# Optimization experiments

Hardware: AMD Instinct MI355X
Metric: run time of the kernel (lower is better)

The kernel has to match this reference:

```python
import jax, jax.numpy as jnp
import numpy as np

EPS = 1e-5

def layernorm(x, w, b):
    mu = jnp.mean(x, axis=-1, keepdims=True)
    xc = x - mu
    var = jnp.mean(xc * xc, axis=-1, keepdims=True)
    return xc * jax.lax.rsqrt(var + EPS) * w + b

def setup_inputs() -> dict:
    key = jax.random.key(0)
    ks = jax.random.split(key, 9)
    B, T, Nm, Nl = 8, 8, 1024, 64
    Vw, Tw, H, Dh = 1024, 2048, 8, 64
    inner = H * Dh  # 512
    s_q = 1.0 / np.sqrt(Tw)
    s_kv = 1.0 / np.sqrt(Vw)
    s_o = 1.0 / np.sqrt(inner)
    return {
        "x": jax.random.normal(ks[0], (B, T, Nm, Vw), jnp.float32),
        "latents": jax.random.normal(ks[1], (B, T, Nl, Tw), jnp.float32),
        "nm_w": jnp.ones((Vw,), jnp.float32),
        "nm_b": jnp.zeros((Vw,), jnp.float32),
        "nl_w": jnp.ones((Tw,), jnp.float32),
        "nl_b": jnp.zeros((Tw,), jnp.float32),
        "Wq": jax.random.normal(ks[2], (Tw, inner), jnp.float32) * s_q,
        "Wkv": jax.random.normal(ks[3], (Vw, 2 * inner), jnp.float32) * s_kv,
        "Wout": jax.random.normal(ks[4], (inner, Tw), jnp.float32) * s_o,
    }

def reference(x, latents, nm_w, nm_b, nl_w, nl_b, Wq, Wkv, Wout):
    H, Dh = 8, 64
    scale = Dh ** (-0.5)
    B, T, Nm, _ = x.shape
    Nl = latents.shape[2]
    xn = layernorm(x, nm_w, nm_b)          # (B,T,Nm,Vw)
    ln = layernorm(latents, nl_w, nl_b)    # (B,T,Nl,Tw)
    q = (ln @ Wq).reshape(B, T, Nl, H, Dh)           # b t i h d
    kv = xn @ Wkv                                     # (B,T,Nm,2*inner)
    k, v = jnp.split(kv, 2, axis=-1)
    k = k.reshape(B, T, Nm, H, Dh)                    # b t j h d
    v = v.reshape(B, T, Nm, H, Dh)
    sim = jnp.einsum('btihd,btjhd->bthij', q * scale, k)  # (B,T,H,Nl,Nm)
    attn = jax.nn.softmax(sim, axis=-1)
    out = jnp.einsum('bthij,btjhd->btihd', attn, v)       # (B,T,Nl,H,Dh)
    out = out.reshape(B, T, Nl, H * Dh)
    return out @ Wout                                     # (B,T,Nl,Tw)
```

## Files before the change

kernel.cpp:

```cpp
#include <hip/hip_runtime.h>

typedef __attribute__((ext_vector_type(8))) short bfrag8;
typedef __attribute__((ext_vector_type(4))) float f32x4;

typedef const unsigned int __attribute__((address_space(1)))* gas1_u32;
typedef unsigned int __attribute__((address_space(3)))* gas3_u32;

#define DEV __device__ __forceinline__

DEV unsigned short f2bf(float f) {
  unsigned int u = __builtin_bit_cast(unsigned int, f);
  u += 0x7fffu + ((u >> 16) & 1u);
  return (unsigned short)(u >> 16);
}

DEV void gload_lds16(const void* g, void* l) {
  __builtin_amdgcn_global_load_lds((gas1_u32)g, (gas3_u32)l, 16, 0, 0);
}

__global__ __launch_bounds__(256) void k_xstats(
    const float* __restrict__ x, unsigned short* __restrict__ xb,
    float* __restrict__ mu, float* __restrict__ rstd)
{
  const int wid = threadIdx.x >> 6, lane = threadIdx.x & 63;
  const int row = blockIdx.x * 4 + wid;
  const float* base = x + (size_t)row * 1024;
  float4 v[4];
  #pragma unroll
  for (int i = 0; i < 4; ++i) v[i] = ((const float4*)base)[i * 64 + lane];
  float s = 0.f, q = 0.f;
  #pragma unroll
  for (int i = 0; i < 4; ++i) {
    s += v[i].x + v[i].y + v[i].z + v[i].w;
    q += v[i].x*v[i].x + v[i].y*v[i].y + v[i].z*v[i].z + v[i].w*v[i].w;
  }
  #pragma unroll
  for (int off = 32; off >= 1; off >>= 1) { s += __shfl_xor(s, off); q += __shfl_xor(q, off); }
  const float m  = s * (1.0f/1024.0f);
  const float var = q * (1.0f/1024.0f) - m * m;
  const float rs = rsqrtf(var + 1e-5f);
  if (lane == 0) { mu[row] = m; rstd[row] = rs; }
  unsigned short* ob = xb + (size_t)row * 1024;
  #pragma unroll
  for (int i = 0; i < 4; ++i) {
    ushort4 o;
    o.x = f2bf(v[i].x); o.y = f2bf(v[i].y); o.z = f2bf(v[i].z); o.w = f2bf(v[i].w);
    ((ushort4*)ob)[i * 64 + lane] = o;
  }
}

__global__ __launch_bounds__(256) void k_lnlat(
    const float* __restrict__ lat, const float* __restrict__ w,
    const float* __restrict__ b, unsigned short* __restrict__ ln)
{
  const int row = blockIdx.x, tid = threadIdx.x;
  const float* base = lat + (size_t)row * 2048;
  const float4 v0 = ((const float4*)base)[tid];
  const float4 v1 = ((const float4*)base)[256 + tid];
  float s = v0.x+v0.y+v0.z+v0.w + v1.x+v1.y+v1.z+v1.w;
  float q = v0.x*v0.x+v0.y*v0.y+v0.z*v0.z+v0.w*v0.w
          + v1.x*v1.x+v1.y*v1.y+v1.z*v1.z+v1.w*v1.w;
  #pragma unroll
  for (int off = 32; off >= 1; off >>= 1) { s += __shfl_xor(s, off); q += __shfl_xor(q, off); }
  __shared__ float red[8];
  const int wid = tid >> 6, lane = tid & 63;
  if (lane == 0) { red[wid] = s; red[4 + wid] = q; }
  __syncthreads();
  s = red[0] + red[1] + red[2] + red[3];
  q = red[4] + red[5] + red[6] + red[7];
  const float m  = s * (1.0f/2048.0f);
  const float var = q * (1.0f/2048.0f) - m * m;
  const float rs = rsqrtf(var + 1e-5f);
  const float4 w0 = ((const float4*)w)[tid], w1 = ((const float4*)w)[256 + tid];
  const float4 b0 = ((const float4*)b)[tid], b1 = ((const float4*)b)[256 + tid];
  ushort4 o0, o1;
  o0.x = f2bf((v0.x - m) * rs * w0.x + b0.x);
  o0.y = f2bf((v0.y - m) * rs * w0.y + b0.y);
  o0.z = f2bf((v0.z - m) * rs * w0.z + b0.z);
  o0.w = f2bf((v0.w - m) * rs * w0.w + b0.w);
  o1.x = f2bf((v1.x - m) * rs * w1.x + b1.x);
  o1.y = f2bf((v1.y - m) * rs * w1.y + b1.y);
  o1.z = f2bf((v1.z - m) * rs * w1.z + b1.z);
  o1.w = f2bf((v1.w - m) * rs * w1.w + b1.w);
  ((ushort4*)(ln + (size_t)row * 2048))[tid] = o0;
  ((ushort4*)(ln + (size_t)row * 2048))[256 + tid] = o1;
}

__global__ __launch_bounds__(256) void k_transpose_cast(
    const float* __restrict__ src, unsigned short* __restrict__ dst,
    int K, int N, const float* __restrict__ rowscale, float scale)
{
  __shared__ float tile[32][33];
  const int tx = threadIdx.x & 31, ty = threadIdx.x >> 5;
  const int ntiles = N >> 5;
  const int k0 = (blockIdx.x / ntiles) << 5;
  const int n0 = (blockIdx.x % ntiles) << 5;
  #pragma unroll
  for (int r = 0; r < 4; ++r) {
    const int kk = ty + r * 8;
    float v = src[(size_t)(k0 + kk) * N + n0 + tx] * scale;
    if (rowscale) v *= rowscale[k0 + kk];
    tile[kk][tx] = v;
  }
  __syncthreads();
  #pragma unroll
  for (int r = 0; r < 4; ++r) {
    const int nn = ty + r * 8;
    dst[(size_t)(n0 + nn) * K + k0 + tx] = f2bf(tile[tx][nn]);
  }
}

__global__ __launch_bounds__(256) void k_c1c2_part(
    const float* __restrict__ Wkv, const float* __restrict__ w,
    const float* __restrict__ b, float* __restrict__ part)
{
  const int kc = blockIdx.x;
  const int n  = blockIdx.y * 256 + threadIdx.x;
  float s1 = 0.f, s2 = 0.f;
  const int k0 = kc * 64;
  for (int k = k0; k < k0 + 64; ++k) {
    const float wv = Wkv[(size_t)k * 1024 + n];
    s1 += w[k] * wv;
    s2 += b[k] * wv;
  }
  part[(size_t)(kc * 2 + 0) * 1024 + n] = s1;
  part[(size_t)(kc * 2 + 1) * 1024 + n] = s2;
}

__global__ __launch_bounds__(256) void k_c1c2_red(
    const float* __restrict__ part, float* __restrict__ c1, float* __restrict__ c2)
{
  const int n = blockIdx.x * 256 + threadIdx.x;
  float s1 = 0.f, s2 = 0.f;
  #pragma unroll
  for (int kc = 0; kc < 16; ++kc) {
    s1 += part[(size_t)(kc * 2 + 0) * 1024 + n];
    s2 += part[(size_t)(kc * 2 + 1) * 1024 + n];
  }
  c1[n] = s1; c2[n] = s2;
}

template<int BM, int BN, int BK, int WM, int WN, int NT, int MODE>
__global__ __launch_bounds__(NT, 2) void k_gemm(
    const unsigned short* __restrict__ A, int lda,
    const unsigned short* __restrict__ Bt, int ldb,
    int Mb, int K, int mtiles, int ntiles,
    void* __restrict__ Cout, int ldc,
    const float* __restrict__ mu, const float* __restrict__ rstd,
    const float* __restrict__ c1, const float* __restrict__ c2)
{
  static_assert(BK == 64, "staging/swizzle assumes BK=64 (128B rows)");
  constexpr int NW = NT / 64;
  constexpr int MF = (BM / WM) / 16;
  constexpr int NF = (BN / WN) / 16;
  constexpr int KS = BK / 32;
  constexpr int LA = (BM * BK) / (8 * NT);
  constexpr int LB = (BN * BK) / (8 * NT);
  static_assert(WM * WN == NW, "wave grid");

  __shared__ __attribute__((aligned(16))) unsigned short As0[BM * BK];
  __shared__ __attribute__((aligned(16))) unsigned short As1[BM * BK];
  __shared__ __attribute__((aligned(16))) unsigned short Bs0[BN * BK];
  __shared__ __attribute__((aligned(16))) unsigned short Bs1[BN * BK];

  int bid = blockIdx.x;
  {
    const int nwg = gridDim.x;
    if ((nwg & 7) == 0) {
      const int q = nwg >> 3;
      bid = (bid & 7) * q + (bid >> 3);
    }
  }
  const int per_bt = mtiles * ntiles;
  const int bt = bid / per_bt;
  const int r  = bid % per_bt;
  const int mt = r / ntiles, nt = r % ntiles;
  const int tid = threadIdx.x;
  const int wid = tid >> 6, lane = tid & 63;
  const int g = lane >> 4, c = lane & 15;
  const int wr = wid / WN, wc = wid % WN;
  const int MO = wr * (BM / WM), NO = wc * (BN / WN);

  const size_t abase = ((size_t)bt * Mb + (size_t)mt * BM) * lda;
  const size_t bbase = (size_t)nt * BN * (size_t)ldb;

  const f32x4 zz = {0.f, 0.f, 0.f, 0.f};
  f32x4 acc[MF][NF];
  #pragma unroll
  for (int m = 0; m < MF; ++m)
    #pragma unroll
    for (int n = 0; n < NF; ++n) acc[m][n] = zz;

  auto stage = [&](unsigned short* da, unsigned short* db, int kt) {
    const unsigned short* ga = A + abase + (size_t)kt * BK;
    #pragma unroll
    for (int i = 0; i < LA; ++i) {
      const int o = (i * NT + tid) * 16;
      const int row = o >> 7;
      const int colb = (o & 127) ^ ((row & 3) << 5);
      gload_lds16((const char*)(ga + (size_t)row * lda) + colb, (char*)da + o);
    }
    const unsigned short* gb = Bt + bbase + (size_t)kt * BK;
    #pragma unroll
    for (int i = 0; i < LB; ++i) {
      const int o = (i * NT + tid) * 16;
      const int row = o >> 7;
      const int colb = (o & 127) ^ ((row & 3) << 5);
      gload_lds16((const char*)(gb + (size_t)row * ldb) + colb, (char*)db + o);
    }
  };

  auto compute = [&](const unsigned short* as, const unsigned short* bs) {
    #pragma unroll
    for (int kk = 0; kk < KS; ++kk) {
      bfrag8 af[MF], bf[NF];
      #pragma unroll
      for (int m = 0; m < MF; ++m) {
        const int rw = MO + m * 16 + c;
        af[m] = *(const bfrag8*)((const char*)as + rw * (BK * 2)
                                 + ((kk * 64 + g * 16) ^ ((rw & 3) << 5)));
      }
      #pragma unroll
      for (int n = 0; n < NF; ++n) {
        const int rw = NO + n * 16 + c;
        bf[n] = *(const bfrag8*)((const char*)bs + rw * (BK * 2)
                                 + ((kk * 64 + g * 16) ^ ((rw & 3) << 5)));
      }
      #pragma unroll
      for (int m = 0; m < MF; ++m)
        #pragma unroll
        for (int n = 0; n < NF; ++n)
          acc[m][n] = __builtin_amdgcn_mfma_f32_16x16x32_bf16(af[m], bf[n], acc[m][n], 0, 0, 0);
    }
  };

  const int nkt = K / BK;
  stage(As0, Bs0, 0);
  __syncthreads();
  for (int kt = 0; kt < nkt; kt += 2) {
    if (kt + 1 < nkt) stage(As1, Bs1, kt + 1);
    compute(As0, Bs0);
    __syncthreads();
    if (kt + 2 < nkt) stage(As0, Bs0, kt + 2);
    if (kt + 1 < nkt) compute(As1, Bs1);
    __syncthreads();
  }

  #pragma unroll
  for (int m = 0; m < MF; ++m) {
    #pragma unroll
    for (int j = 0; j < 4; ++j) {
      const int grow = mt * BM + MO + m * 16 + g * 4 + j;
      const size_t orow = (size_t)bt * Mb + grow;
      float rs = 0.f, muv = 0.f;
      if constexpr (MODE == 0) { rs = rstd[orow]; muv = mu[orow]; }
      #pragma unroll
      for (int n = 0; n < NF; ++n) {
        const int gcol = nt * BN + NO + n * 16 + c;
        float v = acc[m][n][j];
        if constexpr (MODE == 0) v = rs * (v - muv * c1[gcol]) + c2[gcol];
        if constexpr (MODE == 2) ((float*)Cout)[orow * ldc + gcol] = v;
        else ((unsigned short*)Cout)[orow * ldc + gcol] = f2bf(v);
      }
    }
  }
}

__global__ __launch_bounds__(256) void k_attn(
    const unsigned short* __restrict__ q,
    const unsigned short* __restrict__ kv,
    unsigned short* __restrict__ ao)
{
  __shared__ __attribute__((aligned(16))) unsigned short Vt[64 * 64];
  const int bid = blockIdx.x;
  const int bt = bid >> 3, h = bid & 7;
  const int tid = threadIdx.x;
  const int wid = tid >> 6, lane = tid & 63;
  const int g = lane >> 4, c = lane & 15;

  const size_t qoff = ((size_t)bt * 64 + wid * 16 + c) * 512 + h * 64;
  const bfrag8 qf0 = *(const bfrag8*)(q + qoff + g * 8);
  const bfrag8 qf1 = *(const bfrag8*)(q + qoff + 32 + g * 8);

  const f32x4 zz = {0.f, 0.f, 0.f, 0.f};
  f32x4 o[4] = {zz, zz, zz, zz};
  float m_run = -1e30f, l_run = 0.f;

  const size_t kvbase = (size_t)bt * 1024 * 1024;
  const unsigned short* kbase = kv + kvbase + h * 64;
  const unsigned short* vbase = kv + kvbase + 512 + h * 64;

  for (int ch = 0; ch < 16; ++ch) {
    #pragma unroll
    for (int rr = 0; rr < 2; ++rr) {
      const int key = rr * 32 + (tid >> 3);
      const int d0 = (tid & 7) * 8;
      const bfrag8 vv = *(const bfrag8*)(vbase + (size_t)(ch * 64 + key) * 1024 + d0);
      #pragma unroll
      for (int j = 0; j < 8; ++j)
        Vt[(d0 + j) * 64 + (key ^ (j << 3))] = (unsigned short)vv[j];
    }
    __syncthreads();
    #pragma unroll
    for (int ks = 0; ks < 2; ++ks) {
      const int kb = ch * 64 + ks * 32;
      f32x4 s[2];
      #pragma unroll
      for (int t = 0; t < 2; ++t) {
        const int kr = ((c >> 2) << 3) + (t << 2) + (c & 3);
        const unsigned short* krow = kbase + (size_t)(kb + kr) * 1024;
        s[t] = zz;
        s[t] = __builtin_amdgcn_mfma_f32_16x16x32_bf16(*(const bfrag8*)(krow + g * 8),      qf0, s[t], 0, 0, 0);
        s[t] = __builtin_amdgcn_mfma_f32_16x16x32_bf16(*(const bfrag8*)(krow + 32 + g * 8), qf1, s[t], 0, 0, 0);
      }
      float pm = s[0][0];
      #pragma unroll
      for (int i = 1; i < 4; ++i) pm = fmaxf(pm, s[0][i]);
      #pragma unroll
      for (int i = 0; i < 4; ++i) pm = fmaxf(pm, s[1][i]);
      pm = fmaxf(pm, __shfl_xor(pm, 16));
      pm = fmaxf(pm, __shfl_xor(pm, 32));
      const float mn = fmaxf(m_run, pm);
      const float alpha = __expf(m_run - mn);
      float p[8];
      #pragma unroll
      for (int i = 0; i < 4; ++i) p[i]     = __expf(s[0][i] - mn);
      #pragma unroll
      for (int i = 0; i < 4; ++i) p[4 + i] = __expf(s[1][i] - mn);
      float ts = 0.f;
      #pragma unroll
      for (int i = 0; i < 8; ++i) ts += p[i];
      ts += __shfl_xor(ts, 16);
      ts += __shfl_xor(ts, 32);
      l_run = l_run * alpha + ts;
      m_run = mn;
      float ar[4];
      #pragma unroll
      for (int rj = 0; rj < 4; ++rj) ar[rj] = __shfl(alpha, g * 4 + rj);
      #pragma unroll
      for (int db = 0; db < 4; ++db)
        #pragma unroll
        for (int j = 0; j < 4; ++j) o[db][j] *= ar[j];
      bfrag8 pa;
      #pragma unroll
      for (int i = 0; i < 8; ++i) pa[i] = (short)f2bf(p[i]);
      #pragma unroll
      for (int db = 0; db < 4; ++db) {
        const int d = db * 16 + c;
        const bfrag8 vb = *(const bfrag8*)(Vt + d * 64 + ((ks * 32 + g * 8) ^ ((c & 7) << 3)));
        o[db] = __builtin_amdgcn_mfma_f32_16x16x32_bf16(pa, vb, o[db], 0, 0, 0);
      }
    }
    __syncthreads();
  }
  float lr[4];
  #pragma unroll
  for (int rj = 0; rj < 4; ++rj) lr[rj] = __shfl(l_run, g * 4 + rj);
  #pragma unroll
  for (int db = 0; db < 4; ++db)
    #pragma unroll
    for (int j = 0; j < 4; ++j) {
      const float val = o[db][j] / lr[j];
      ao[((size_t)bt * 64 + wid * 16 + g * 4 + j) * 512 + h * 64 + db * 16 + c] = f2bf(val);
    }
}

extern "C" void kernel_launch(void* const* d_in, const int* in_sizes, int n_in,
                              void* d_out, int out_size, void* d_ws, size_t ws_size,
                              hipStream_t stream)
{
  const float* x    = (const float*)d_in[0];
  const float* lat  = (const float*)d_in[1];
  const float* nm_w = (const float*)d_in[2];
  const float* nm_b = (const float*)d_in[3];
  const float* nl_w = (const float*)d_in[4];
  const float* nl_b = (const float*)d_in[5];
  const float* Wq   = (const float*)d_in[6];
  const float* Wkv  = (const float*)d_in[7];
  const float* Wout = (const float*)d_in[8];

  char* p = (char*)d_ws;
  auto take = [&](size_t bytes) { char* r = p; p += (bytes + 255) & ~(size_t)255; return r; };
  unsigned short* xb    = (unsigned short*)take(64ull * 1024 * 1024 * 2);
  unsigned short* kvb   = (unsigned short*)take(64ull * 1024 * 1024 * 2);
  unsigned short* lnb   = (unsigned short*)take(4096ull * 2048 * 2);
  unsigned short* qbuf  = (unsigned short*)take(4096ull * 512 * 2);
  unsigned short* aob   = (unsigned short*)take(4096ull * 512 * 2);
  unsigned short* WqT   = (unsigned short*)take(512ull * 2048 * 2);
  unsigned short* WkvT  = (unsigned short*)take(1024ull * 1024 * 2);
  unsigned short* WoutT = (unsigned short*)take(2048ull * 512 * 2);
  float* muv  = (float*)take(65536ull * 4);
  float* rsd  = (float*)take(65536ull * 4);
  float* c1   = (float*)take(1024 * 4);
  float* c2   = (float*)take(1024 * 4);
  float* part = (float*)take(32ull * 1024 * 4);
  if ((size_t)(p - (char*)d_ws) > ws_size) return;

  k_transpose_cast<<<dim3(64 * 16), 256, 0, stream>>>(Wq,   WqT,   2048,  512, nullptr, 0.125f);
  k_transpose_cast<<<dim3(32 * 32), 256, 0, stream>>>(Wkv,  WkvT,  1024, 1024, nm_w,    1.0f);
  k_transpose_cast<<<dim3(16 * 64), 256, 0, stream>>>(Wout, WoutT,  512, 2048, nullptr, 1.0f);
  k_c1c2_part<<<dim3(16, 4), 256, 0, stream>>>(Wkv, nm_w, nm_b, part);
  k_c1c2_red<<<dim3(4), 256, 0, stream>>>(part, c1, c2);
  k_xstats<<<dim3(16384), 256, 0, stream>>>(x, xb, muv, rsd);
  k_lnlat<<<dim3(4096), 256, 0, stream>>>(lat, nl_w, nl_b, lnb);

  k_gemm<256, 256, 64, 2, 4, 512, 0><<<dim3(1024), 512, 0, stream>>>(
      xb, 1024, WkvT, 1024, 1024, 1024, 4, 4, kvb, 1024, muv, rsd, c1, c2);
  k_gemm<64, 128, 64, 1, 4, 256, 1><<<dim3(256), 256, 0, stream>>>(
      lnb, 2048, WqT, 2048, 64, 2048, 1, 4, qbuf, 512, nullptr, nullptr, nullptr, nullptr);

  k_attn<<<dim3(512), 256, 0, stream>>>(qbuf, kvb, aob);

  k_gemm<64, 128, 64, 1, 4, 256, 2><<<dim3(1024), 256, 0, stream>>>(
      aob, 512, WoutT, 512, 64, 512, 1, 16, d_out, 2048, nullptr, nullptr, nullptr, nullptr);
}
```

Before: 375.2 us.

## Rework GEMM into 4-stage BK=32 ring pipeline with single barrier and rotated swizzle

```diff
diff --git a/kernel.cpp b/kernel.cpp
--- a/kernel.cpp
+++ b/kernel.cpp
@@ -140,28 +140,28 @@
   c1[n] = s1; c2[n] = s2;
 }
 
-template<int BM, int BN, int BK, int WM, int WN, int NT, int MODE>
+template<int BM, int BN, int WM, int WN, int NT, int MODE>
 __global__ __launch_bounds__(NT, 2) void k_gemm(
     const unsigned short* __restrict__ A, int lda,
     const unsigned short* __restrict__ Bt, int ldb,
-    int Mb, int K, int mtiles, int ntiles,
+    int K, int mtiles, int ntiles,
     void* __restrict__ Cout, int ldc,
     const float* __restrict__ mu, const float* __restrict__ rstd,
     const float* __restrict__ c1, const float* __restrict__ c2)
 {
-  static_assert(BK == 64, "staging/swizzle assumes BK=64 (128B rows)");
+  constexpr int BK = 32;
   constexpr int NW = NT / 64;
   constexpr int MF = (BM / WM) / 16;
   constexpr int NF = (BN / WN) / 16;
-  constexpr int KS = BK / 32;
   constexpr int LA = (BM * BK) / (8 * NT);
   constexpr int LB = (BN * BK) / (8 * NT);
+  constexpr int RA = BM * BK;
+  constexpr int RB = BN * BK;
   static_assert(WM * WN == NW, "wave grid");
-
-  __shared__ __attribute__((aligned(16))) unsigned short As0[BM * BK];
-  __shared__ __attribute__((aligned(16))) unsigned short As1[BM * BK];
-  __shared__ __attribute__((aligned(16))) unsigned short Bs0[BN * BK];
-  __shared__ __attribute__((aligned(16))) unsigned short Bs1[BN * BK];
+  static_assert(LA >= 1 && LB >= 1, "tile too small for NT");
+
+  __shared__ __attribute__((aligned(16))) unsigned short As[4 * RA];
+  __shared__ __attribute__((aligned(16))) unsigned short Bs[4 * RB];
 
   int bid = blockIdx.x;
   {
@@ -171,18 +171,16 @@
       bid = (bid & 7) * q + (bid >> 3);
     }
   }
-  const int per_bt = mtiles * ntiles;
-  const int bt = bid / per_bt;
-  const int r  = bid % per_bt;
-  const int mt = r / ntiles, nt = r % ntiles;
+  const int mt = bid / ntiles, nt = bid % ntiles;
   const int tid = threadIdx.x;
   const int wid = tid >> 6, lane = tid & 63;
   const int g = lane >> 4, c = lane & 15;
   const int wr = wid / WN, wc = wid % WN;
   const int MO = wr * (BM / WM), NO = wc * (BN / WN);
-
-  const size_t abase = ((size_t)bt * Mb + (size_t)mt * BM) * lda;
-  const size_t bbase = (size_t)nt * BN * (size_t)ldb;
+  const int rot = (c >> 1) & 3;
+
+  const unsigned short* gA = A + (size_t)mt * BM * lda;
+  const unsigned short* gB = Bt + (size_t)nt * BN * ldb;
 
   const f32x4 zz = {0.f, 0.f, 0.f, 0.f};
   f32x4 acc[MF][NF];
@@ -191,67 +189,65 @@
     #pragma unroll
     for (int n = 0; n < NF; ++n) acc[m][n] = zz;
 
-  auto stage = [&](unsigned short* da, unsigned short* db, int kt) {
-    const unsigned short* ga = A + abase + (size_t)kt * BK;
+  auto stage = [&](int R, int kt) {
     #pragma unroll
     for (int i = 0; i < LA; ++i) {
       const int o = (i * NT + tid) * 16;
-      const int row = o >> 7;
-      const int colb = (o & 127) ^ ((row & 3) << 5);
-      gload_lds16((const char*)(ga + (size_t)row * lda) + colb, (char*)da + o);
-    }
-    const unsigned short* gb = Bt + bbase + (size_t)kt * BK;
+      const int row = o >> 6;
+      const int slot = (o >> 4) & 3;
+      const int srcb = (((slot - ((row >> 1) & 3)) & 3) << 4);
+      gload_lds16((const char*)(gA + (size_t)row * lda + kt * BK) + srcb,
+                  (char*)(As + R * RA) + o);
+    }
     #pragma unroll
     for (int i = 0; i < LB; ++i) {
       const int o = (i * NT + tid) * 16;
-      const int row = o >> 7;
-      const int colb = (o & 127) ^ ((row & 3) << 5);
-      gload_lds16((const char*)(gb + (size_t)row * ldb) + colb, (char*)db + o);
+      const int row = o >> 6;
+      const int slot = (o >> 4) & 3;
+      const int srcb = (((slot - ((row >> 1) & 3)) & 3) << 4);
+      gload_lds16((const char*)(gB + (size_t)row * ldb + kt * BK) + srcb,
+                  (char*)(Bs + R * RB) + o);
     }
   };
 
-  auto compute = [&](const unsigned short* as, const unsigned short* bs) {
-    #pragma unroll
-    for (int kk = 0; kk < KS; ++kk) {
-      bfrag8 af[MF], bf[NF];
-      #pragma unroll
-      for (int m = 0; m < MF; ++m) {
-        const int rw = MO + m * 16 + c;
-        af[m] = *(const bfrag8*)((const char*)as + rw * (BK * 2)
-                                 + ((kk * 64 + g * 16) ^ ((rw & 3) << 5)));
-      }
-      #pragma unroll
-      for (int n = 0; n < NF; ++n) {
-        const int rw = NO + n * 16 + c;
-        bf[n] = *(const bfrag8*)((const char*)bs + rw * (BK * 2)
-                                 + ((kk * 64 + g * 16) ^ ((rw & 3) << 5)));
-      }
-      #pragma unroll
-      for (int m = 0; m < MF; ++m)
-        #pragma unroll
-        for (int n = 0; n < NF; ++n)
-          acc[m][n] = __builtin_amdgcn_mfma_f32_16x16x32_bf16(af[m], bf[n], acc[m][n], 0, 0, 0);
-    }
+  auto compute = [&](int R) {
+    const char* as = (const char*)(As + R * RA);
+    const char* bs = (const char*)(Bs + R * RB);
+    bfrag8 af[MF], bf[NF];
+    #pragma unroll
+    for (int m = 0; m < MF; ++m) {
+      const int rw = MO + m * 16 + c;
+      af[m] = *(const bfrag8*)(as + rw * 64 + (((g + rot) & 3) << 4));
+    }
+    #pragma unroll
+    for (int n = 0; n < NF; ++n) {
+      const int rw = NO + n * 16 + c;
+      bf[n] = *(const bfrag8*)(bs + rw * 64 + (((g + rot) & 3) << 4));
+    }
+    #pragma unroll
+    for (int m = 0; m < MF; ++m)
+      #pragma unroll
+      for (int n = 0; n < NF; ++n)
+        acc[m][n] = __builtin_amdgcn_mfma_f32_16x16x32_bf16(af[m], bf[n], acc[m][n], 0, 0, 0);
   };
 
   const int nkt = K / BK;
-  stage(As0, Bs0, 0);
-  __syncthreads();
-  for (int kt = 0; kt < nkt; kt += 2) {
-    if (kt + 1 < nkt) stage(As1, Bs1, kt + 1);
-    compute(As0, Bs0);
-    __syncthreads();
-    if (kt + 2 < nkt) stage(As0, Bs0, kt + 2);
-    if (kt + 1 < nkt) compute(As1, Bs1);
-    __syncthreads();
+  stage(0, 0); stage(1, 1); stage(2, 2);
+  for (int t = 0; t < nkt; t += 4) {
+    #pragma unroll
+    for (int r = 0; r < 4; ++r) {
+      int t3 = t + r + 3; if (t3 >= nkt) t3 -= nkt;
+      asm volatile("s_waitcnt vmcnt(8)\n\ts_barrier" ::: "memory");
+      stage((r + 3) & 3, t3);
+      compute(r);
+    }
   }
 
   #pragma unroll
   for (int m = 0; m < MF; ++m) {
     #pragma unroll
     for (int j = 0; j < 4; ++j) {
-      const int grow = mt * BM + MO + m * 16 + g * 4 + j;
-      const size_t orow = (size_t)bt * Mb + grow;
+      const size_t orow = (size_t)mt * BM + MO + m * 16 + g * 4 + j;
       float rs = 0.f, muv = 0.f;
       if constexpr (MODE == 0) { rs = rstd[orow]; muv = mu[orow]; }
       #pragma unroll
@@ -404,13 +400,13 @@
   k_xstats<<<dim3(16384), 256, 0, stream>>>(x, xb, muv, rsd);
   k_lnlat<<<dim3(4096), 256, 0, stream>>>(lat, nl_w, nl_b, lnb);
 
-  k_gemm<256, 256, 64, 2, 4, 512, 0><<<dim3(1024), 512, 0, stream>>>(
-      xb, 1024, WkvT, 1024, 1024, 1024, 4, 4, kvb, 1024, muv, rsd, c1, c2);
-  k_gemm<64, 128, 64, 1, 4, 256, 1><<<dim3(256), 256, 0, stream>>>(
-      lnb, 2048, WqT, 2048, 64, 2048, 1, 4, qbuf, 512, nullptr, nullptr, nullptr, nullptr);
+  k_gemm<256, 256, 2, 4, 512, 0><<<dim3(1024), 512, 0, stream>>>(
+      xb, 1024, WkvT, 1024, 1024, 256, 4, kvb, 1024, muv, rsd, c1, c2);
+  k_gemm<128, 128, 2, 2, 256, 1><<<dim3(128), 256, 0, stream>>>(
+      lnb, 2048, WqT, 2048, 2048, 32, 4, qbuf, 512, nullptr, nullptr, nullptr, nullptr);
 
   k_attn<<<dim3(512), 256, 0, stream>>>(qbuf, kvb, aob);
 
-  k_gemm<64, 128, 64, 1, 4, 256, 2><<<dim3(1024), 256, 0, stream>>>(
-      aob, 512, WoutT, 512, 64, 512, 1, 16, d_out, 2048, nullptr, nullptr, nullptr, nullptr);
-}
+  k_gemm<128, 128, 2, 2, 256, 2><<<dim3(512), 256, 0, stream>>>(
+      aob, 512, WoutT, 512, 512, 32, 16, d_out, 2048, nullptr, nullptr, nullptr, nullptr);
+}
```

Result: slower. 388.9 us (+3.6%).
